# Kernel tuning notes

Measured on AMD Instinct MI355X. Metric: run time of the kernel, lower is better.

## Reference

```python
import jax, jax.numpy as jnp
import numpy as np

N = 4096          # batch of MNIST images
K = 2             # kernel size
NW = K * K        # 4 wires
DIM = 2 ** NW     # 16-dim statevector
NP_ = (28 // K) ** 2  # 196 patches per image


def setup_inputs() -> dict:
    key = jax.random.key(0)
    kx, kw = jax.random.split(key, 2)
    # pixel angles in [0, pi] for the RY encoder
    x = jax.random.uniform(kx, (N, 1, 28, 28), dtype=jnp.float32) * np.float32(np.pi)
    # fixed Haar-random 16x16 unitary standing in for the RandomLayer circuit
    rng = np.random.default_rng(0)
    A = rng.normal(size=(DIM, DIM)) + 1j * rng.normal(size=(DIM, DIM))
    Q, R = np.linalg.qr(A)
    d = np.diagonal(R)
    Q = Q * (d / np.abs(d))  # phase-fix -> Haar unitary
    U_re = jnp.asarray(Q.real, dtype=jnp.float32)
    U_im = jnp.asarray(Q.imag, dtype=jnp.float32)
    # linear head params (kaiming-ish small init)
    W = jax.random.normal(kw, (10, NP_ * NW), dtype=jnp.float32) * 0.02
    b = jnp.zeros((10,), dtype=jnp.float32)
    return {"x": x, "U_re": U_re, "U_im": U_im, "W": W, "b": b}


def reference(x, U_re, U_im, W, b):
    n = x.shape[0]
    # unfold into 2x2 non-overlapping patches, row-major pixels per patch -> [n*196, 4]
    p = x.reshape(n, 14, K, 14, K).transpose(0, 1, 3, 2, 4).reshape(n * NP_, NW)
    half = p * 0.5
    # RY(theta) on |0> -> [cos(theta/2), sin(theta/2)] per wire (real amplitudes)
    v = jnp.stack([jnp.cos(half), jnp.sin(half)], axis=-1)  # [P, 4, 2]
    # product state psi[b0 b1 b2 b3] (wire 0 = most significant bit) -> [P, 16]
    psi = jnp.einsum('pa,pb,pc,pd->pabcd', v[:, 0], v[:, 1], v[:, 2], v[:, 3]).reshape(-1, DIM)
    # random-layer unitary
    U = U_re + 1j * U_im
    phi = psi.astype(U.dtype) @ U.T                        # [P, 16] complex
    probs = jnp.real(phi * jnp.conj(phi))                  # [P, 16]
    # PauliZ expectation per wire: +1 if that bit is 0 else -1
    idx = jnp.arange(DIM)
    shifts = jnp.arange(NW - 1, -1, -1)                    # wire k <-> bit (3-k)
    signs = (1.0 - 2.0 * ((idx[:, None] >> shifts[None, :]) & 1)).astype(probs.dtype)  # [16, 4]
    z = probs @ signs                                      # [P, 4]
    feats = z.reshape(n, NP_ * NW)                         # [n, 784]
    logits = feats @ W.T + b
    return jax.nn.log_softmax(logits, axis=-1)
```

## Files before the change

### kernel.cpp

```cpp
#include <hip/hip_runtime.h>
#include <math.h>

using bf16x8 = __attribute__((ext_vector_type(8))) short;
using f32x4  = __attribute__((ext_vector_type(4))) float;

static __device__ __forceinline__ unsigned cvt_pk_bf16(float lo, float hi) {
    unsigned r;
    asm("v_cvt_pk_bf16_f32 %0, %1, %2" : "=v"(r) : "v"(lo), "v"(hi));
    return r;
}
static __device__ __forceinline__ unsigned short f2bf(float f) {
    union { float f; unsigned u; } v; v.f = f;
    unsigned r = v.u + 0x7FFFu + ((v.u >> 16) & 1u);
    return (unsigned short)(r >> 16);
}

#define REV_HALF 0.07957747154594767f

static __device__ __forceinline__ void sincos_half(float theta, float* s, float* c) {
    const float r = theta * REV_HALF;
    *s = __builtin_amdgcn_sinf(r);
    *c = __builtin_amdgcn_cosf(r);
}

__global__ __launch_bounds__(256) void quanv_one(
    const float* __restrict__ x,
    const float* __restrict__ U_re,
    const float* __restrict__ U_im,
    const float* __restrict__ W,
    const float* __restrict__ bias,
    float* __restrict__ out)
{
    __shared__ uint4  psiQ[4][64][4];
    __shared__ float4 sfeat4[196];
    __shared__ float  slog[10];

    const int tid  = threadIdx.x;
    const int wv   = tid >> 6;
    const int lane = tid & 63;
    const int img  = blockIdx.x;

    bf16x8 uaRe, uaIm;
    if (lane < 32) {
        const int row = lane & 15, kb = (lane >> 4) * 8;
        const float4* pr4 = (const float4*)(U_re + row * 16 + kb);
        const float4* pi4 = (const float4*)(U_im + row * 16 + kb);
        const float4 r0 = pr4[0], r1 = pr4[1], i0 = pi4[0], i1 = pi4[1];
        uaRe[0] = (short)f2bf(r0.x); uaRe[1] = (short)f2bf(r0.y);
        uaRe[2] = (short)f2bf(r0.z); uaRe[3] = (short)f2bf(r0.w);
        uaRe[4] = (short)f2bf(r1.x); uaRe[5] = (short)f2bf(r1.y);
        uaRe[6] = (short)f2bf(r1.z); uaRe[7] = (short)f2bf(r1.w);
        uaIm[0] = (short)f2bf(i0.x); uaIm[1] = (short)f2bf(i0.y);
        uaIm[2] = (short)f2bf(i0.z); uaIm[3] = (short)f2bf(i0.w);
        uaIm[4] = (short)f2bf(i1.x); uaIm[5] = (short)f2bf(i1.y);
        uaIm[6] = (short)f2bf(i1.z); uaIm[7] = (short)f2bf(i1.w);
    } else {
        #pragma unroll
        for (int i = 0; i < 8; ++i) { uaRe[i] = 0; uaIm[i] = 0; }
    }

    const int p   = (tid < 196) ? tid : 195;
    const int prw = p / 14;
    const int pcl = p - prw * 14;
    const float* xi = x + (size_t)img * 784 + prw * 56 + pcl * 2;
    const float2 t0 = *(const float2*)xi;
    const float2 t1 = *(const float2*)(xi + 28);
    float s0, c0, s1, c1, s2, c2, s3, c3;
    sincos_half(t0.x, &s0, &c0);
    sincos_half(t0.y, &s1, &c1);
    sincos_half(t1.x, &s2, &c2);
    sincos_half(t1.y, &s3, &c3);
    const float a0 = c0 * c1, a1 = c0 * s1, a2 = s0 * c1, a3 = s0 * s1;
    const float b0 = c2 * c3, b1 = c2 * s3, b2 = s2 * c3, b3 = s2 * s3;

    uint4 lo, hi;
    lo.x = cvt_pk_bf16(a0 * b0, a0 * b1); lo.y = cvt_pk_bf16(a0 * b2, a0 * b3);
    lo.z = cvt_pk_bf16(a1 * b0, a1 * b1); lo.w = cvt_pk_bf16(a1 * b2, a1 * b3);
    hi.x = cvt_pk_bf16(a2 * b0, a2 * b1); hi.y = cvt_pk_bf16(a2 * b2, a2 * b3);
    hi.z = cvt_pk_bf16(a3 * b0, a3 * b1); hi.w = cvt_pk_bf16(a3 * b2, a3 * b3);

    const int sw_w = (lane ^ (lane >> 2)) & 3;
    const uint4 z4 = make_uint4(0u, 0u, 0u, 0u);
    psiQ[wv][lane][0 ^ sw_w] = lo;
    psiQ[wv][lane][1 ^ sw_w] = hi;
    psiQ[wv][lane][2 ^ sw_w] = z4;
    psiQ[wv][lane][3 ^ sw_w] = z4;
    __syncthreads();

    const int g    = lane >> 4;
    const int cpat = lane & 15;
    const f32x4 zacc = {0.f, 0.f, 0.f, 0.f};

    #pragma unroll
    for (int T = 0; T < 4; ++T) {
        const int row = T * 16 + cpat;
        const int sw_r = (row ^ (row >> 2)) & 3;
        const bf16x8 bfrag = *(const bf16x8*)&psiQ[wv][row][g ^ sw_r];
        const f32x4 dre = __builtin_amdgcn_mfma_f32_16x16x32_bf16(uaRe, bfrag, zacc, 0, 0, 0);
        const f32x4 dim = __builtin_amdgcn_mfma_f32_16x16x32_bf16(uaIm, bfrag, zacc, 0, 0, 0);
        const float P0 = dre[0] * dre[0] + dim[0] * dim[0];
        const float P1 = dre[1] * dre[1] + dim[1] * dim[1];
        const float P2 = dre[2] * dre[2] + dim[2] * dim[2];
        const float P3 = dre[3] * dre[3] + dim[3] * dim[3];
        float S  = P0 + P1 + P2 + P3;
        float B2 = P0 + P1 - P2 - P3;
        float B3 = P0 - P1 + P2 - P3;
        B2 += __shfl_xor(B2, 16, 64); B2 += __shfl_xor(B2, 32, 64);
        B3 += __shfl_xor(B3, 16, 64); B3 += __shfl_xor(B3, 32, 64);
        const float t16 = __shfl_xor(S, 16, 64);
        float d = (g & 1) ? (t16 - S) : (S - t16);
        const float e = S + t16;
        d += __shfl_xor(d, 32, 64);
        const float t32 = __shfl_xor(e, 32, 64);
        const float z0 = (g & 2) ? (t32 - e) : (e - t32);
        const int sp = wv * 64 + T * 16 + cpat;
        if (lane < 16 && sp < 196) {
            sfeat4[sp] = make_float4(z0, d, B2, B3);
        }
    }
    __syncthreads();

    const float* sfeat = (const float*)sfeat4;
    const int cs = (wv == 0) ? 0 : (wv == 1) ? 3 : (wv == 2) ? 6 : 8;
    const int nc = (wv <= 1) ? 3 : 2;
    float acc0 = 0.f, acc1 = 0.f, acc2 = 0.f;
    #pragma unroll
    for (int i = 0; i < 12; ++i) {
        const int f = i * 64 + lane;
        const float fv = sfeat[f];
        acc0 = fmaf(W[(cs + 0) * 784 + f], fv, acc0);
        acc1 = fmaf(W[(cs + 1) * 784 + f], fv, acc1);
        if (nc > 2) acc2 = fmaf(W[(cs + 2) * 784 + f], fv, acc2);
    }
    if (lane < 16) {
        const int f = 768 + lane;
        const float fv = sfeat[f];
        acc0 = fmaf(W[(cs + 0) * 784 + f], fv, acc0);
        acc1 = fmaf(W[(cs + 1) * 784 + f], fv, acc1);
        if (nc > 2) acc2 = fmaf(W[(cs + 2) * 784 + f], fv, acc2);
    }
    #pragma unroll
    for (int off = 32; off; off >>= 1) {
        acc0 += __shfl_xor(acc0, off, 64);
        acc1 += __shfl_xor(acc1, off, 64);
        acc2 += __shfl_xor(acc2, off, 64);
    }
    if (lane == 0) {
        slog[cs + 0] = acc0 + bias[cs + 0];
        slog[cs + 1] = acc1 + bias[cs + 1];
        if (nc > 2) slog[cs + 2] = acc2 + bias[cs + 2];
    }
    __syncthreads();

    if (wv == 0 && lane < 16) {
        const float lg = (lane < 10) ? slog[lane] : -1e30f;
        float m = lg;
        #pragma unroll
        for (int off = 8; off; off >>= 1) m = fmaxf(m, __shfl_xor(m, off, 64));
        float e = (lane < 10) ? __expf(lg - m) : 0.f;
        float s = e;
        #pragma unroll
        for (int off = 8; off; off >>= 1) s += __shfl_xor(s, off, 64);
        if (lane < 10) out[(size_t)img * 10 + lane] = lg - m - __logf(s);
    }
}

extern "C" void kernel_launch(void* const* d_in, const int* in_sizes, int n_in,
                              void* d_out, int out_size, void* d_ws, size_t ws_size,
                              hipStream_t stream) {
    const float* x    = (const float*)d_in[0];
    const float* U_re = (const float*)d_in[1];
    const float* U_im = (const float*)d_in[2];
    const float* W    = (const float*)d_in[3];
    const float* bias = (const float*)d_in[4];
    float* out = (float*)d_out;
    const int n = in_sizes[0] / 784;
    quanv_one<<<n, 256, 0, stream>>>(x, U_re, U_im, W, bias, out);
}
```

Baseline: 21.14 us.

## Use 32x32x16 MFMA with stacked Re/Im rows and register-shuffled psi operands

```diff
diff --git a/kernel.cpp b/kernel.cpp
--- a/kernel.cpp
+++ b/kernel.cpp
@@ -2,26 +2,15 @@
 #include <math.h>
 
 using bf16x8 = __attribute__((ext_vector_type(8))) short;
-using f32x4  = __attribute__((ext_vector_type(4))) float;
+using f32x16 = __attribute__((ext_vector_type(16))) float;
 
 static __device__ __forceinline__ unsigned cvt_pk_bf16(float lo, float hi) {
     unsigned r;
     asm("v_cvt_pk_bf16_f32 %0, %1, %2" : "=v"(r) : "v"(lo), "v"(hi));
     return r;
 }
-static __device__ __forceinline__ unsigned short f2bf(float f) {
-    union { float f; unsigned u; } v; v.f = f;
-    unsigned r = v.u + 0x7FFFu + ((v.u >> 16) & 1u);
-    return (unsigned short)(r >> 16);
-}
 
 #define REV_HALF 0.07957747154594767f
-
-static __device__ __forceinline__ void sincos_half(float theta, float* s, float* c) {
-    const float r = theta * REV_HALF;
-    *s = __builtin_amdgcn_sinf(r);
-    *c = __builtin_amdgcn_cosf(r);
-}
 
 __global__ __launch_bounds__(256) void quanv_one(
     const float* __restrict__ x,
@@ -31,33 +20,24 @@
     const float* __restrict__ bias,
     float* __restrict__ out)
 {
-    __shared__ uint4  psiQ[4][64][4];
     __shared__ float4 sfeat4[196];
     __shared__ float  slog[10];
 
     const int tid  = threadIdx.x;
     const int wv   = tid >> 6;
     const int lane = tid & 63;
+    const int l31  = lane & 31;
+    const int hi   = lane >> 5;
     const int img  = blockIdx.x;
 
-    bf16x8 uaRe, uaIm;
-    if (lane < 32) {
-        const int row = lane & 15, kb = (lane >> 4) * 8;
-        const float4* pr4 = (const float4*)(U_re + row * 16 + kb);
-        const float4* pi4 = (const float4*)(U_im + row * 16 + kb);
-        const float4 r0 = pr4[0], r1 = pr4[1], i0 = pi4[0], i1 = pi4[1];
-        uaRe[0] = (short)f2bf(r0.x); uaRe[1] = (short)f2bf(r0.y);
-        uaRe[2] = (short)f2bf(r0.z); uaRe[3] = (short)f2bf(r0.w);
-        uaRe[4] = (short)f2bf(r1.x); uaRe[5] = (short)f2bf(r1.y);
-        uaRe[6] = (short)f2bf(r1.z); uaRe[7] = (short)f2bf(r1.w);
-        uaIm[0] = (short)f2bf(i0.x); uaIm[1] = (short)f2bf(i0.y);
-        uaIm[2] = (short)f2bf(i0.z); uaIm[3] = (short)f2bf(i0.w);
-        uaIm[4] = (short)f2bf(i1.x); uaIm[5] = (short)f2bf(i1.y);
-        uaIm[6] = (short)f2bf(i1.z); uaIm[7] = (short)f2bf(i1.w);
-    } else {
-        #pragma unroll
-        for (int i = 0; i < 8; ++i) { uaRe[i] = 0; uaIm[i] = 0; }
-    }
+    const float* Urow = (l31 < 16) ? (U_re + l31 * 16) : (U_im + (l31 - 16) * 16);
+    const float4 uf0 = *(const float4*)(Urow + hi * 8);
+    const float4 uf1 = *(const float4*)(Urow + hi * 8 + 4);
+    union { unsigned u[4]; bf16x8 v; } ua;
+    ua.u[0] = cvt_pk_bf16(uf0.x, uf0.y);
+    ua.u[1] = cvt_pk_bf16(uf0.z, uf0.w);
+    ua.u[2] = cvt_pk_bf16(uf1.x, uf1.y);
+    ua.u[3] = cvt_pk_bf16(uf1.z, uf1.w);
 
     const int p   = (tid < 196) ? tid : 195;
     const int prw = p / 14;
@@ -65,57 +45,64 @@
     const float* xi = x + (size_t)img * 784 + prw * 56 + pcl * 2;
     const float2 t0 = *(const float2*)xi;
     const float2 t1 = *(const float2*)(xi + 28);
-    float s0, c0, s1, c1, s2, c2, s3, c3;
-    sincos_half(t0.x, &s0, &c0);
-    sincos_half(t0.y, &s1, &c1);
-    sincos_half(t1.x, &s2, &c2);
-    sincos_half(t1.y, &s3, &c3);
+    const float r0 = t0.x * REV_HALF, r1 = t0.y * REV_HALF;
+    const float r2 = t1.x * REV_HALF, r3 = t1.y * REV_HALF;
+    const float s0 = __builtin_amdgcn_sinf(r0), c0 = __builtin_amdgcn_cosf(r0);
+    const float s1 = __builtin_amdgcn_sinf(r1), c1 = __builtin_amdgcn_cosf(r1);
+    const float s2 = __builtin_amdgcn_sinf(r2), c2 = __builtin_amdgcn_cosf(r2);
+    const float s3 = __builtin_amdgcn_sinf(r3), c3 = __builtin_amdgcn_cosf(r3);
     const float a0 = c0 * c1, a1 = c0 * s1, a2 = s0 * c1, a3 = s0 * s1;
     const float b0 = c2 * c3, b1 = c2 * s3, b2 = s2 * c3, b3 = s2 * s3;
 
-    uint4 lo, hi;
-    lo.x = cvt_pk_bf16(a0 * b0, a0 * b1); lo.y = cvt_pk_bf16(a0 * b2, a0 * b3);
-    lo.z = cvt_pk_bf16(a1 * b0, a1 * b1); lo.w = cvt_pk_bf16(a1 * b2, a1 * b3);
-    hi.x = cvt_pk_bf16(a2 * b0, a2 * b1); hi.y = cvt_pk_bf16(a2 * b2, a2 * b3);
-    hi.z = cvt_pk_bf16(a3 * b0, a3 * b1); hi.w = cvt_pk_bf16(a3 * b2, a3 * b3);
+    unsigned pL[4], pH[4];
+    pL[0] = cvt_pk_bf16(a0 * b0, a0 * b1); pL[1] = cvt_pk_bf16(a0 * b2, a0 * b3);
+    pL[2] = cvt_pk_bf16(a1 * b0, a1 * b1); pL[3] = cvt_pk_bf16(a1 * b2, a1 * b3);
+    pH[0] = cvt_pk_bf16(a2 * b0, a2 * b1); pH[1] = cvt_pk_bf16(a2 * b2, a2 * b3);
+    pH[2] = cvt_pk_bf16(a3 * b0, a3 * b1); pH[3] = cvt_pk_bf16(a3 * b2, a3 * b3);
 
-    const int sw_w = (lane ^ (lane >> 2)) & 3;
-    const uint4 z4 = make_uint4(0u, 0u, 0u, 0u);
-    psiQ[wv][lane][0 ^ sw_w] = lo;
-    psiQ[wv][lane][1 ^ sw_w] = hi;
-    psiQ[wv][lane][2 ^ sw_w] = z4;
-    psiQ[wv][lane][3 ^ sw_w] = z4;
-    __syncthreads();
-
-    const int g    = lane >> 4;
-    const int cpat = lane & 15;
-    const f32x4 zacc = {0.f, 0.f, 0.f, 0.f};
+    f32x16 zacc;
+    #pragma unroll
+    for (int i = 0; i < 16; ++i) zacc[i] = 0.f;
 
     #pragma unroll
-    for (int T = 0; T < 4; ++T) {
-        const int row = T * 16 + cpat;
-        const int sw_r = (row ^ (row >> 2)) & 3;
-        const bf16x8 bfrag = *(const bf16x8*)&psiQ[wv][row][g ^ sw_r];
-        const f32x4 dre = __builtin_amdgcn_mfma_f32_16x16x32_bf16(uaRe, bfrag, zacc, 0, 0, 0);
-        const f32x4 dim = __builtin_amdgcn_mfma_f32_16x16x32_bf16(uaIm, bfrag, zacc, 0, 0, 0);
-        const float P0 = dre[0] * dre[0] + dim[0] * dim[0];
-        const float P1 = dre[1] * dre[1] + dim[1] * dim[1];
-        const float P2 = dre[2] * dre[2] + dim[2] * dim[2];
-        const float P3 = dre[3] * dre[3] + dim[3] * dim[3];
-        float S  = P0 + P1 + P2 + P3;
-        float B2 = P0 + P1 - P2 - P3;
-        float B3 = P0 - P1 + P2 - P3;
-        B2 += __shfl_xor(B2, 16, 64); B2 += __shfl_xor(B2, 32, 64);
-        B3 += __shfl_xor(B3, 16, 64); B3 += __shfl_xor(B3, 32, 64);
-        const float t16 = __shfl_xor(S, 16, 64);
-        float d = (g & 1) ? (t16 - S) : (S - t16);
-        const float e = S + t16;
-        d += __shfl_xor(d, 32, 64);
-        const float t32 = __shfl_xor(e, 32, 64);
-        const float z0 = (g & 2) ? (t32 - e) : (e - t32);
-        const int sp = wv * 64 + T * 16 + cpat;
-        if (lane < 16 && sp < 196) {
-            sfeat4[sp] = make_float4(z0, d, B2, B3);
+    for (int T = 0; T < 2; ++T) {
+        union { unsigned u[4]; bf16x8 v; } pb;
+        #pragma unroll
+        for (int c = 0; c < 4; ++c) {
+            if (T == 0) {
+                const unsigned sw = (unsigned)__shfl_xor((int)pH[c], 32, 64);
+                pb.u[c] = hi ? sw : pL[c];
+            } else {
+                const unsigned sw = (unsigned)__shfl_xor((int)pL[c], 32, 64);
+                pb.u[c] = hi ? pH[c] : sw;
+            }
+        }
+
+        const f32x16 d = __builtin_amdgcn_mfma_f32_32x32x16_bf16(ua.v, pb.v, zacc, 0, 0, 0);
+
+        float P[8];
+        #pragma unroll
+        for (int r = 0; r < 8; ++r) P[r] = fmaf(d[r], d[r], d[r + 8] * d[r + 8]);
+
+        const float u0 = P[0] + P[1], u1 = P[0] - P[1];
+        const float u2 = P[2] + P[3], u3 = P[2] - P[3];
+        const float v0 = P[4] + P[5], v1 = P[4] - P[5];
+        const float v2 = P[6] + P[7], v3 = P[6] - P[7];
+        const float tpp0 = u0 + u2, tb1_0 = u0 - u2, tb0_0 = u1 + u3;
+        const float tpp1 = v0 + v2, tb1_1 = v0 - v2, tb0_1 = v1 + v3;
+        const float S   = tpp0 + tpp1;
+        const float z0p = tpp0 - tpp1;
+        const float z2p = tb1_0 + tb1_1;
+        const float z3p = tb0_0 + tb0_1;
+        const float Sx = __shfl_xor(S, 32, 64);
+        const float z0 = z0p + __shfl_xor(z0p, 32, 64);
+        const float z2 = z2p + __shfl_xor(z2p, 32, 64);
+        const float z3 = z3p + __shfl_xor(z3p, 32, 64);
+        const float z1 = hi ? (Sx - S) : (S - Sx);
+
+        if (!hi) {
+            const int sp = wv * 64 + T * 32 + l31;
+            if (sp < 196) sfeat4[sp] = make_float4(z0, z1, z2, z3);
         }
     }
     __syncthreads();
```

Result: faster. 18.30 us (-13.4%).
